# Kernel optimization log

Hardware: AMD Instinct MI355X
Metric: run time of the kernel (lower is better)

The kernel has to match this reference:

```python
import jax, jax.numpy as jnp
import numpy as np

ZETA = 1.1
GAMMA = -0.1

B, F, D = 1024, 32, 128


def setup_inputs() -> dict:
    key = jax.random.key(0)
    k1, k2 = jax.random.split(key)
    feature = jax.random.normal(k1, (B, F, D), dtype=jnp.float32)
    # nn.Parameter init: normal(mean=0, std=0.001)
    matrix = jax.random.normal(k2, (F, F, D, D), dtype=jnp.float32) * 0.001
    return {"feature": feature, "matrix": matrix}


def reference(feature, matrix):
    # feature: [B, F, D]; matrix (logAlpha of hard-concrete gate): [F, F, D, D]
    nF = matrix.shape[0]
    # strict upper-triangular pair mask over (i, j)
    mask = jnp.triu(jnp.ones((nF, nF), dtype=feature.dtype), k=1)
    # deterministic (eval-mode) hard-concrete gate: stretch + clamp
    s = jax.nn.sigmoid(matrix)
    z = jnp.clip(s * (ZETA - GAMMA) + GAMMA, 0.0, 1.0)
    l0_out = mask[:, :, None, None] * z  # [F, F, D, D]
    # out[b,i,j] = f_i^T Z_ij f_j  == sum_{d,e} f[b,i,d] * Z[i,j,d,e] * f[b,j,e]
    # (faithful to: (f[:, :, None, :, None] @ f[:, None, :, None, :]) * Z, summed over (d, e))
    out = jnp.einsum('bid,ijde,bje->bij', feature, l0_out, feature)
    return out
```

## Files before the change

kernel.cpp:

```cpp
#include <hip/hip_runtime.h>

#define B_SZ 1024
#define F_SZ 32
#define D_SZ 128
#define FD   (F_SZ * D_SZ)
#define LDA  136
#define LDB  136

typedef __bf16 bf16x8 __attribute__((ext_vector_type(8)));
typedef float floatx4 __attribute__((ext_vector_type(4)));

__device__ __forceinline__ unsigned short f2bf(float f) {
  unsigned u = __float_as_uint(f);
  u += 0x7fffu + ((u >> 16) & 1u);
  return (unsigned short)(u >> 16);
}

__device__ __forceinline__ float bf2f(unsigned short h) {
  return __uint_as_float(((unsigned)h) << 16);
}

__global__ __launch_bounds__(256, 2)
void interaction_pair_kernel(const float* __restrict__ feat,
                             const float* __restrict__ mat,
                             float* __restrict__ out) {
  __shared__ unsigned short sA[128 * LDA];
  __shared__ unsigned short sBT[128 * LDB];

  const int t    = threadIdx.x;
  const int w    = t >> 6;
  const int lane = t & 63;
  const int l15  = lane & 15;
  const int quad = lane >> 4;

  int p = blockIdx.x;
  int i = 0;
  while (p >= F_SZ - 1 - i) { p -= F_SZ - 1 - i; ++i; }
  const int j = i + 1 + p;

  {
    const float* zp = mat + (((size_t)i * F_SZ + j) * (size_t)(D_SZ * D_SZ));
    #pragma unroll 8
    for (int it = 0; it < 64; ++it) {
      int idx = it * 256 + t;
      int d = idx >> 7, e = idx & 127;
      float v = zp[idx];
      float s = 1.0f / (1.0f + __expf(-v));
      float z = fminf(1.0f, fmaxf(0.0f, fmaf(s, 1.2f, -0.1f)));
      sBT[e * LDB + d] = f2bf(z);
    }
  }

  for (int bt = 0; bt < 8; ++bt) {
    const int b0 = bt * 128;

    #pragma unroll 4
    for (int it = 0; it < 16; ++it) {
      int idx4 = it * 256 + t;
      int r = idx4 >> 5, c4 = idx4 & 31;
      const float4 v = *(const float4*)(feat + (size_t)(b0 + r) * FD + i * D_SZ + c4 * 4);
      ushort4 h;
      h.x = f2bf(v.x); h.y = f2bf(v.y); h.z = f2bf(v.z); h.w = f2bf(v.w);
      *(ushort4*)(&sA[r * LDA + c4 * 4]) = h;
    }
    __syncthreads();

    floatx4 acc[2][8];
    #pragma unroll
    for (int mf = 0; mf < 2; ++mf)
      #pragma unroll
      for (int nf = 0; nf < 8; ++nf)
        acc[mf][nf] = (floatx4){0.f, 0.f, 0.f, 0.f};

    #pragma unroll
    for (int k0 = 0; k0 < 128; k0 += 32) {
      const int kc = k0 + quad * 8;
      bf16x8 a0 = *(const bf16x8*)&sA[(w * 32 +      l15) * LDA + kc];
      bf16x8 a1 = *(const bf16x8*)&sA[(w * 32 + 16 + l15) * LDA + kc];
      #pragma unroll
      for (int nf = 0; nf < 8; ++nf) {
        bf16x8 bfr = *(const bf16x8*)&sBT[(nf * 16 + l15) * LDB + kc];
        acc[0][nf] = __builtin_amdgcn_mfma_f32_16x16x32_bf16(a0, bfr, acc[0][nf], 0, 0, 0);
        acc[1][nf] = __builtin_amdgcn_mfma_f32_16x16x32_bf16(a1, bfr, acc[1][nf], 0, 0, 0);
      }
    }

    #pragma unroll
    for (int mf = 0; mf < 2; ++mf) {
      float pl[4] = {0.f, 0.f, 0.f, 0.f};
      const int rb = w * 32 + mf * 16 + quad * 4;
      #pragma unroll
      for (int nf = 0; nf < 8; ++nf) {
        const int col = nf * 16 + l15;
        const float* fj = feat + (size_t)(b0 + rb) * FD + j * D_SZ + col;
        floatx4 c = acc[mf][nf];
        pl[0] += c[0] * fj[0];
        pl[1] += c[1] * fj[FD];
        pl[2] += c[2] * fj[2 * FD];
        pl[3] += c[3] * fj[3 * FD];
      }
      #pragma unroll
      for (int off = 1; off < 16; off <<= 1) {
        pl[0] += __shfl_xor(pl[0], off, 64);
        pl[1] += __shfl_xor(pl[1], off, 64);
        pl[2] += __shfl_xor(pl[2], off, 64);
        pl[3] += __shfl_xor(pl[3], off, 64);
      }
      if (l15 == 0) {
        size_t ob = (size_t)(b0 + rb) * (F_SZ * F_SZ) + (size_t)i * F_SZ + j;
        out[ob]                    = pl[0];
        out[ob + 1 * F_SZ * F_SZ]  = pl[1];
        out[ob + 2 * F_SZ * F_SZ]  = pl[2];
        out[ob + 3 * F_SZ * F_SZ]  = pl[3];
      }
    }
    __syncthreads();
  }
}

extern "C" void kernel_launch(void* const* d_in, const int* in_sizes, int n_in,
                              void* d_out, int out_size, void* d_ws, size_t ws_size,
                              hipStream_t stream) {
  const float* feat = (const float*)d_in[0];
  const float* mat  = (const float*)d_in[1];
  float* out = (float*)d_out;

  hipMemsetAsync(out, 0, (size_t)out_size * sizeof(float), stream);

  const int n_pairs = F_SZ * (F_SZ - 1) / 2;
  interaction_pair_kernel<<<dim3(n_pairs), dim3(256), 0, stream>>>(feat, mat, out);
}
```

Before: 145.7 us.

## Precompute bf16 features and swizzled gate matrix, split batch across four blocks per pair

Moves the fp32-to-bf16 feature conversion and the sigmoid/clamp/transpose of the gate matrix into separate prep kernels that write to workspace. The main kernel splits each pair's batch into four blocks, loads the pre-swizzled Z tile into LDS with direct global-to-LDS loads, and keeps Z fragments in registers. A-operand fragments are read straight from global bf16 features, and the per-tile syncs are removed. This raises the grid from 496 blocks to 1984, cutting redundant conversion work and per-block serial latency. The cost is two extra launches, workspace traffic, and higher register pressure from holding all Z fragments.

```diff
diff --git a/kernel.cpp b/kernel.cpp
--- a/kernel.cpp
+++ b/kernel.cpp
@@ -4,11 +4,12 @@
 #define F_SZ 32
 #define D_SZ 128
 #define FD   (F_SZ * D_SZ)
-#define LDA  136
-#define LDB  136
+#define NPAIR 496
 
 typedef __bf16 bf16x8 __attribute__((ext_vector_type(8)));
 typedef float floatx4 __attribute__((ext_vector_type(4)));
+typedef unsigned short u16x4 __attribute__((ext_vector_type(4)));
+typedef unsigned short u16x8 __attribute__((ext_vector_type(8)));
 
 __device__ __forceinline__ unsigned short f2bf(float f) {
   unsigned u = __float_as_uint(f);
@@ -16,16 +17,69 @@
   return (unsigned short)(u >> 16);
 }
 
-__device__ __forceinline__ float bf2f(unsigned short h) {
-  return __uint_as_float(((unsigned)h) << 16);
+__device__ __forceinline__ void gload_lds16(const void* g, void* l) {
+  __builtin_amdgcn_global_load_lds(
+      (const __attribute__((address_space(1))) unsigned int*)g,
+      (__attribute__((address_space(3))) unsigned int*)l,
+      16, 0, 0);
+}
+
+__global__ void feat_cvt_kernel(const float* __restrict__ feat,
+                                unsigned short* __restrict__ featB) {
+  const int idx8 = blockIdx.x * 256 + threadIdx.x;
+  const float4* f4 = (const float4*)feat;
+  const float4 v0 = f4[(size_t)idx8 * 2];
+  const float4 v1 = f4[(size_t)idx8 * 2 + 1];
+  u16x8 h;
+  h[0] = f2bf(v0.x); h[1] = f2bf(v0.y); h[2] = f2bf(v0.z); h[3] = f2bf(v0.w);
+  h[4] = f2bf(v1.x); h[5] = f2bf(v1.y); h[6] = f2bf(v1.z); h[7] = f2bf(v1.w);
+  *(u16x8*)&featB[(size_t)idx8 * 8] = h;
+}
+
+__global__ void z_prep_kernel(const float* __restrict__ mat,
+                              unsigned short* __restrict__ ZT) {
+  __shared__ unsigned short tr[128 * 132];
+  const int t = threadIdx.x;
+
+  int p = blockIdx.x, i = 0;
+  while (p >= F_SZ - 1 - i) { p -= F_SZ - 1 - i; ++i; }
+  const int j = i + 1 + p;
+
+  const float* zp = mat + (((size_t)i * F_SZ + j) * (size_t)(D_SZ * D_SZ));
+  #pragma unroll 4
+  for (int it = 0; it < 16; ++it) {
+    int idx4 = it * 256 + t;
+    int d = idx4 >> 5, e4 = (idx4 & 31) * 4;
+    const float4 v = *(const float4*)(zp + d * D_SZ + e4);
+    float zs[4] = {v.x, v.y, v.z, v.w};
+    #pragma unroll
+    for (int c = 0; c < 4; ++c) {
+      float s = 1.0f / (1.0f + __expf(-zs[c]));
+      float z = fminf(1.0f, fmaxf(0.0f, fmaf(s, 1.2f, -0.1f)));
+      tr[(e4 + c) * 132 + d] = f2bf(z);
+    }
+  }
+  __syncthreads();
+
+  unsigned short* zo = ZT + (size_t)blockIdx.x * (D_SZ * D_SZ);
+  #pragma unroll 2
+  for (int it = 0; it < 8; ++it) {
+    int G = it * 256 + t;
+    int e = G >> 4, gp = G & 15;
+    int g = gp ^ (e & 7);
+    u16x4 lo = *(const u16x4*)&tr[e * 132 + g * 8];
+    u16x4 hi = *(const u16x4*)&tr[e * 132 + g * 8 + 4];
+    *(u16x4*)&zo[e * 128 + gp * 8]     = lo;
+    *(u16x4*)&zo[e * 128 + gp * 8 + 4] = hi;
+  }
 }
 
 __global__ __launch_bounds__(256, 2)
 void interaction_pair_kernel(const float* __restrict__ feat,
-                             const float* __restrict__ mat,
+                             const unsigned short* __restrict__ featB,
+                             const unsigned short* __restrict__ ZT,
                              float* __restrict__ out) {
-  __shared__ unsigned short sA[128 * LDA];
-  __shared__ unsigned short sBT[128 * LDB];
+  __shared__ unsigned short sZ[128 * 128];
 
   const int t    = threadIdx.x;
   const int w    = t >> 6;
@@ -33,37 +87,36 @@
   const int l15  = lane & 15;
   const int quad = lane >> 4;
 
-  int p = blockIdx.x;
-  int i = 0;
+  const int pid   = blockIdx.x >> 2;
+  const int split = blockIdx.x & 3;
+  int p = pid, i = 0;
   while (p >= F_SZ - 1 - i) { p -= F_SZ - 1 - i; ++i; }
   const int j = i + 1 + p;
 
   {
-    const float* zp = mat + (((size_t)i * F_SZ + j) * (size_t)(D_SZ * D_SZ));
-    #pragma unroll 8
-    for (int it = 0; it < 64; ++it) {
-      int idx = it * 256 + t;
-      int d = idx >> 7, e = idx & 127;
-      float v = zp[idx];
-      float s = 1.0f / (1.0f + __expf(-v));
-      float z = fminf(1.0f, fmaxf(0.0f, fmaf(s, 1.2f, -0.1f)));
-      sBT[e * LDB + d] = f2bf(z);
+    const char* src = (const char*)(ZT + (size_t)pid * (D_SZ * D_SZ));
+    #pragma unroll
+    for (int it = 0; it < 8; ++it) {
+      int off = it * 4096 + w * 1024;
+      gload_lds16(src + off + lane * 16, (char*)sZ + off);
     }
   }
+  __syncthreads();
 
-  for (int bt = 0; bt < 8; ++bt) {
-    const int b0 = bt * 128;
+  bf16x8 zfr[4][8];
+  #pragma unroll
+  for (int k0 = 0; k0 < 4; ++k0)
+    #pragma unroll
+    for (int nf = 0; nf < 8; ++nf) {
+      const int e    = nf * 16 + l15;
+      const int dcol = k0 * 32 + quad * 8;
+      const int soff = e * 128 + (dcol ^ ((e & 7) << 3));
+      zfr[k0][nf] = *(const bf16x8*)&sZ[soff];
+    }
 
-    #pragma unroll 4
-    for (int it = 0; it < 16; ++it) {
-      int idx4 = it * 256 + t;
-      int r = idx4 >> 5, c4 = idx4 & 31;
-      const float4 v = *(const float4*)(feat + (size_t)(b0 + r) * FD + i * D_SZ + c4 * 4);
-      ushort4 h;
-      h.x = f2bf(v.x); h.y = f2bf(v.y); h.z = f2bf(v.z); h.w = f2bf(v.w);
-      *(ushort4*)(&sA[r * LDA + c4 * 4]) = h;
-    }
-    __syncthreads();
+  const int b0 = split * 256;
+  for (int bt = 0; bt < 2; ++bt) {
+    const int rowbase = b0 + bt * 128 + w * 32;
 
     floatx4 acc[2][8];
     #pragma unroll
@@ -73,26 +126,28 @@
         acc[mf][nf] = (floatx4){0.f, 0.f, 0.f, 0.f};
 
     #pragma unroll
-    for (int k0 = 0; k0 < 128; k0 += 32) {
-      const int kc = k0 + quad * 8;
-      bf16x8 a0 = *(const bf16x8*)&sA[(w * 32 +      l15) * LDA + kc];
-      bf16x8 a1 = *(const bf16x8*)&sA[(w * 32 + 16 + l15) * LDA + kc];
+    for (int mf = 0; mf < 2; ++mf) {
+      bf16x8 af[4];
+      const unsigned short* ap =
+          featB + (size_t)(rowbase + mf * 16 + l15) * FD + i * D_SZ + quad * 8;
       #pragma unroll
-      for (int nf = 0; nf < 8; ++nf) {
-        bf16x8 bfr = *(const bf16x8*)&sBT[(nf * 16 + l15) * LDB + kc];
-        acc[0][nf] = __builtin_amdgcn_mfma_f32_16x16x32_bf16(a0, bfr, acc[0][nf], 0, 0, 0);
-        acc[1][nf] = __builtin_amdgcn_mfma_f32_16x16x32_bf16(a1, bfr, acc[1][nf], 0, 0, 0);
-      }
+      for (int k0 = 0; k0 < 4; ++k0) af[k0] = *(const bf16x8*)(ap + k0 * 32);
+      #pragma unroll
+      for (int k0 = 0; k0 < 4; ++k0)
+        #pragma unroll
+        for (int nf = 0; nf < 8; ++nf)
+          acc[mf][nf] = __builtin_amdgcn_mfma_f32_16x16x32_bf16(
+              af[k0], zfr[k0][nf], acc[mf][nf], 0, 0, 0);
     }
 
     #pragma unroll
     for (int mf = 0; mf < 2; ++mf) {
       float pl[4] = {0.f, 0.f, 0.f, 0.f};
-      const int rb = w * 32 + mf * 16 + quad * 4;
+      const int rb = rowbase + mf * 16 + quad * 4;
       #pragma unroll
       for (int nf = 0; nf < 8; ++nf) {
         const int col = nf * 16 + l15;
-        const float* fj = feat + (size_t)(b0 + rb) * FD + j * D_SZ + col;
+        const float* fj = feat + (size_t)rb * FD + j * D_SZ + col;
         floatx4 c = acc[mf][nf];
         pl[0] += c[0] * fj[0];
         pl[1] += c[1] * fj[FD];
@@ -107,14 +162,13 @@
         pl[3] += __shfl_xor(pl[3], off, 64);
       }
       if (l15 == 0) {
-        size_t ob = (size_t)(b0 + rb) * (F_SZ * F_SZ) + (size_t)i * F_SZ + j;
-        out[ob]                    = pl[0];
-        out[ob + 1 * F_SZ * F_SZ]  = pl[1];
-        out[ob + 2 * F_SZ * F_SZ]  = pl[2];
-        out[ob + 3 * F_SZ * F_SZ]  = pl[3];
+        size_t ob = (size_t)rb * (F_SZ * F_SZ) + (size_t)i * F_SZ + j;
+        out[ob]                   = pl[0];
+        out[ob + 1 * F_SZ * F_SZ] = pl[1];
+        out[ob + 2 * F_SZ * F_SZ] = pl[2];
+        out[ob + 3 * F_SZ * F_SZ] = pl[3];
       }
     }
-    __syncthreads();
   }
 }
 
@@ -125,8 +179,12 @@
   const float* mat  = (const float*)d_in[1];
   float* out = (float*)d_out;
 
+  unsigned short* featB = (unsigned short*)d_ws;
+  unsigned short* ZT    = featB + (size_t)B_SZ * F_SZ * D_SZ;
+
   hipMemsetAsync(out, 0, (size_t)out_size * sizeof(float), stream);
 
-  const int n_pairs = F_SZ * (F_SZ - 1) / 2;
-  interaction_pair_kernel<<<dim3(n_pairs), dim3(256), 0, stream>>>(feat, mat, out);
+  feat_cvt_kernel<<<dim3((B_SZ * F_SZ * D_SZ) / (256 * 8)), dim3(256), 0, stream>>>(feat, featB);
+  z_prep_kernel<<<dim3(NPAIR), dim3(256), 0, stream>>>(mat, ZT);
+  interaction_pair_kernel<<<dim3(NPAIR * 4), dim3(256), 0, stream>>>(feat, featB, ZT, out);
 }
```

New measurement: 155.4 us. +6.7%, slower.

## Split batch across four blocks per pair, fuse zero-fill, swizzle LDS

Applied to the files above, without the earlier changes.

Launches four blocks per (i,j) pair, each covering 256 batch rows, instead of one block looping over all 1024 rows. This raises the grid from 496 to 1984 blocks to fill the GPU better. Each block still recomputes the gate matrix, so the matrix reads and sigmoid work grow fourfold. The separate memset is replaced by having the first 1024 blocks write zeros to the lower-triangle-and-diagonal output entries. The LDS padding is replaced by an XOR swizzle, with the transpose staged through a shared buffer and vectorized float4 matrix loads.

```diff
diff --git a/kernel.cpp b/kernel.cpp
--- a/kernel.cpp
+++ b/kernel.cpp
@@ -3,12 +3,12 @@
 #define B_SZ 1024
 #define F_SZ 32
 #define D_SZ 128
-#define FD   (F_SZ * D_SZ)
-#define LDA  136
-#define LDB  136
+#define FD   4096
+#define NPAIR 496
 
 typedef __bf16 bf16x8 __attribute__((ext_vector_type(8)));
 typedef float floatx4 __attribute__((ext_vector_type(4)));
+typedef unsigned short u16x8 __attribute__((ext_vector_type(8)));
 
 __device__ __forceinline__ unsigned short f2bf(float f) {
   unsigned u = __float_as_uint(f);
@@ -16,16 +16,12 @@
   return (unsigned short)(u >> 16);
 }
 
-__device__ __forceinline__ float bf2f(unsigned short h) {
-  return __uint_as_float(((unsigned)h) << 16);
-}
-
 __global__ __launch_bounds__(256, 2)
-void interaction_pair_kernel(const float* __restrict__ feat,
-                             const float* __restrict__ mat,
-                             float* __restrict__ out) {
-  __shared__ unsigned short sA[128 * LDA];
-  __shared__ unsigned short sBT[128 * LDB];
+void interaction_fused_kernel(const float* __restrict__ feat,
+                              const float* __restrict__ mat,
+                              float* __restrict__ out) {
+  __shared__ unsigned short sZT[128 * 128];
+  __shared__ unsigned short sS[128 * 128];
 
   const int t    = threadIdx.x;
   const int w    = t >> 6;
@@ -33,35 +29,70 @@
   const int l15  = lane & 15;
   const int quad = lane >> 4;
 
-  int p = blockIdx.x;
-  int i = 0;
+  const int bid   = blockIdx.x;
+  const int pid   = bid >> 2;
+  const int split = bid & 3;
+  int p = pid, i = 0;
   while (p >= F_SZ - 1 - i) { p -= F_SZ - 1 - i; ++i; }
   const int j = i + 1 + p;
 
-  {
-    const float* zp = mat + (((size_t)i * F_SZ + j) * (size_t)(D_SZ * D_SZ));
-    #pragma unroll 8
-    for (int it = 0; it < 64; ++it) {
-      int idx = it * 256 + t;
-      int d = idx >> 7, e = idx & 127;
-      float v = zp[idx];
-      float s = 1.0f / (1.0f + __expf(-v));
-      float z = fminf(1.0f, fmaxf(0.0f, fmaf(s, 1.2f, -0.1f)));
-      sBT[e * LDB + d] = f2bf(z);
+  if (bid < B_SZ) {
+    const int ii = t >> 3, s = t & 7;
+    float* ob = out + (size_t)bid * (F_SZ * F_SZ) + ii * F_SZ;
+    #pragma unroll
+    for (int c = 0; c < 4; ++c) {
+      int jj = s * 4 + c;
+      if (jj <= ii) ob[jj] = 0.f;
     }
   }
 
-  for (int bt = 0; bt < 8; ++bt) {
-    const int b0 = bt * 128;
+  {
+    const float* zp = mat + (((size_t)i * F_SZ + j) * (size_t)(D_SZ * D_SZ));
+    #pragma unroll
+    for (int it = 0; it < 16; ++it) {
+      int idx4 = it * 256 + t;
+      int d = idx4 >> 5, e4 = (idx4 & 31) * 4;
+      const float4 v = *(const float4*)(zp + (size_t)d * D_SZ + e4);
+      float zs[4] = {v.x, v.y, v.z, v.w};
+      ushort4 h;
+      unsigned short* hp = &h.x;
+      #pragma unroll
+      for (int c = 0; c < 4; ++c) {
+        float s = 1.0f / (1.0f + __expf(-zs[c]));
+        hp[c] = f2bf(fminf(1.0f, fmaxf(0.0f, fmaf(s, 1.2f, -0.1f))));
+      }
+      *(ushort4*)&sS[d * D_SZ + e4] = h;
+    }
+  }
+  __syncthreads();
 
-    #pragma unroll 4
+  {
+    #pragma unroll
+    for (int it = 0; it < 8; ++it) {
+      int u = it * 256 + t;
+      int e = u & 127, g = u >> 7;
+      u16x8 pk;
+      #pragma unroll
+      for (int r = 0; r < 8; ++r) pk[r] = sS[(g * 8 + r) * D_SZ + e];
+      *(u16x8*)&sZT[e * D_SZ + (g ^ (e & 7)) * 8] = pk;
+    }
+  }
+  __syncthreads();
+
+  #pragma unroll 1
+  for (int pass = 0; pass < 2; ++pass) {
+    const int rbase = split * 256 + pass * 128;
+
+    #pragma unroll
     for (int it = 0; it < 16; ++it) {
       int idx4 = it * 256 + t;
       int r = idx4 >> 5, c4 = idx4 & 31;
-      const float4 v = *(const float4*)(feat + (size_t)(b0 + r) * FD + i * D_SZ + c4 * 4);
+      const float4 v = *(const float4*)(feat + (size_t)(rbase + r) * FD +
+                                        i * D_SZ + c4 * 4);
       ushort4 h;
       h.x = f2bf(v.x); h.y = f2bf(v.y); h.z = f2bf(v.z); h.w = f2bf(v.w);
-      *(ushort4*)(&sA[r * LDA + c4 * 4]) = h;
+      const int grp = c4 >> 1, half8 = (c4 & 1) * 8;
+      *(ushort4*)((char*)sS + r * 256 + ((grp ^ (r & 7)) * 16 + half8)) = h;
     }
     __syncthreads();
 
@@ -72,27 +103,32 @@
       for (int nf = 0; nf < 8; ++nf)
         acc[mf][nf] = (floatx4){0.f, 0.f, 0.f, 0.f};
 
+    const int row0 = w * 32 + l15;
     #pragma unroll
-    for (int k0 = 0; k0 < 128; k0 += 32) {
-      const int kc = k0 + quad * 8;
-      bf16x8 a0 = *(const bf16x8*)&sA[(w * 32 +      l15) * LDA + kc];
-      bf16x8 a1 = *(const bf16x8*)&sA[(w * 32 + 16 + l15) * LDA + kc];
+    for (int k0 = 0; k0 < 4; ++k0) {
+      const int kb = k0 * 64 + quad * 16;
+      bf16x8 a0 = *(const bf16x8*)((const char*)sS + row0 * 256 +
+                                   (kb ^ ((row0 & 7) << 4)));
+      bf16x8 a1 = *(const bf16x8*)((const char*)sS + (row0 + 16) * 256 +
+                                   (kb ^ ((row0 & 7) << 4)));
       #pragma unroll
       for (int nf = 0; nf < 8; ++nf) {
-        bf16x8 bfr = *(const bf16x8*)&sBT[(nf * 16 + l15) * LDB + kc];
-        acc[0][nf] = __builtin_amdgcn_mfma_f32_16x16x32_bf16(a0, bfr, acc[0][nf], 0, 0, 0);
-        acc[1][nf] = __builtin_amdgcn_mfma_f32_16x16x32_bf16(a1, bfr, acc[1][nf], 0, 0, 0);
+        const int e = nf * 16 + l15;
+        bf16x8 bf = *(const bf16x8*)((const char*)sZT + e * 256 +
+                                     (kb ^ ((e & 7) << 4)));
+        acc[0][nf] = __builtin_amdgcn_mfma_f32_16x16x32_bf16(a0, bf, acc[0][nf], 0, 0, 0);
+        acc[1][nf] = __builtin_amdgcn_mfma_f32_16x16x32_bf16(a1, bf, acc[1][nf], 0, 0, 0);
       }
     }
 
     #pragma unroll
     for (int mf = 0; mf < 2; ++mf) {
       float pl[4] = {0.f, 0.f, 0.f, 0.f};
-      const int rb = w * 32 + mf * 16 + quad * 4;
+      const int rg = rbase + w * 32 + mf * 16 + quad * 4;
       #pragma unroll
       for (int nf = 0; nf < 8; ++nf) {
         const int col = nf * 16 + l15;
-        const float* fj = feat + (size_t)(b0 + rb) * FD + j * D_SZ + col;
+        const float* fj = feat + (size_t)rg * FD + j * D_SZ + col;
         floatx4 c = acc[mf][nf];
         pl[0] += c[0] * fj[0];
         pl[1] += c[1] * fj[FD];
@@ -107,11 +143,11 @@
         pl[3] += __shfl_xor(pl[3], off, 64);
       }
       if (l15 == 0) {
-        size_t ob = (size_t)(b0 + rb) * (F_SZ * F_SZ) + (size_t)i * F_SZ + j;
-        out[ob]                    = pl[0];
-        out[ob + 1 * F_SZ * F_SZ]  = pl[1];
-        out[ob + 2 * F_SZ * F_SZ]  = pl[2];
-        out[ob + 3 * F_SZ * F_SZ]  = pl[3];
+        size_t ob = (size_t)rg * (F_SZ * F_SZ) + (size_t)i * F_SZ + j;
+        out[ob]                   = pl[0];
+        out[ob + 1 * F_SZ * F_SZ] = pl[1];
+        out[ob + 2 * F_SZ * F_SZ] = pl[2];
+        out[ob + 3 * F_SZ * F_SZ] = pl[3];
       }
     }
     __syncthreads();
@@ -125,8 +161,5 @@
   const float* mat  = (const float*)d_in[1];
   float* out = (float*)d_out;
 
-  hipMemsetAsync(out, 0, (size_t)out_size * sizeof(float), stream);
-
-  const int n_pairs = F_SZ * (F_SZ - 1) / 2;
-  interaction_pair_kernel<<<dim3(n_pairs), dim3(256), 0, stream>>>(feat, mat, out);
+  interaction_fused_kernel<<<dim3(NPAIR * 4), dim3(256), 0, stream>>>(feat, mat, out);
 }
```

Result: slower. 152.7 us (+4.8%).
